# Kernel tuning notes

Measured on AMD Instinct MI355X. Metric: run time of the kernel, lower is better.

## Reference

```python
import jax, jax.numpy as jnp
import numpy as np

B, H, S, E = 16384, 16, 1, 64
N_OTHERS = 4


def setup_inputs() -> dict:
    key = jax.random.key(0)
    ks = jax.random.split(key, N_OTHERS + 2)
    inp = {f"others_{i}": jax.random.normal(ks[i], (B, H, S, E), dtype=jnp.float32)
           for i in range(N_OTHERS)}
    inp["main"] = jax.random.normal(ks[N_OTHERS], (B, H, S, E), dtype=jnp.float32)
    inp["W"] = jax.random.normal(ks[N_OTHERS + 1], (E, E), dtype=jnp.float32) * (1.0 / np.sqrt(E))
    return inp


def reference(others_0, others_1, others_2, others_3, main, W):
    # mean over the 'others' modalities: (B, H, 1, E)
    mean = (others_0 + others_1 + others_2 + others_3) / 4.0
    m = jnp.squeeze(mean, 2)        # (B, H, E)
    main_sq = jnp.squeeze(main, 2)  # (B, H, E)
    # bilinear score: mean @ W @ main^T -> (B, H, H)
    score = jnp.einsum('bhe,ef,bgf->bhg', m, W, main_sq)
    attn = jax.nn.softmax(score, axis=-1)      # (B, H, H)
    context = jnp.einsum('bhg,bge->bhe', attn, main_sq)  # (B, H, E)
    return context, attn
```

## Files before the change

kernel.cpp:

```cpp
#include <hip/hip_runtime.h>

#define NBATCH 16384
#define H 16
#define E 64
#define NB 4
#define NWAVE 4
#define NBLK (NBATCH / (NB * NWAVE))

#define LGKM0 do { asm volatile("s_waitcnt lgkmcnt(0)" ::: "memory"); \
                   __builtin_amdgcn_sched_barrier(0); } while (0)

__global__ __launch_bounds__(256, 3) void ovo_kernel(
    const float* __restrict__ o0, const float* __restrict__ o1,
    const float* __restrict__ o2, const float* __restrict__ o3,
    const float* __restrict__ mn, const float* __restrict__ W,
    float* __restrict__ ctx_out, float* __restrict__ attn_out)
{
    __shared__ float sW[E * E];
    __shared__ float sT[NWAVE][2][H * 68];

    const int tid = threadIdx.x;
    const int l   = tid & 63;
    const int wv  = tid >> 6;

#pragma unroll
    for (int c = 0; c < 4; ++c) {
        const int idx = c * 1024 + tid * 4;
        *(float4*)&sW[idx] = *(const float4*)&W[idx];
    }
    __syncthreads();

    float* const sA    = &sT[wv][0][0];
    float* const sMain = &sT[wv][1][0];

#pragma unroll 1
    for (int it = 0; it < NB; ++it) {
        const int batch = it * (NBLK * NWAVE) + blockIdx.x * NWAVE + wv;
        const size_t base = (size_t)batch * (H * E);

        float4 ra[4], rb[4], rc[4], rd[4], rv[4];
#pragma unroll
        for (int k = 0; k < 4; ++k) {
            const int off = k * 256 + l * 4;
            ra[k] = *(const float4*)(o0 + base + off);
            rb[k] = *(const float4*)(o1 + base + off);
            rc[k] = *(const float4*)(o2 + base + off);
            rd[k] = *(const float4*)(o3 + base + off);
            rv[k] = *(const float4*)(mn + base + off);
        }

#pragma unroll
        for (int k = 0; k < 4; ++k) {
            const int flat = k * 256 + l * 4;
            const int h = flat >> 6, e = flat & 63;
            float4 m4;
            m4.x = (ra[k].x + rb[k].x + rc[k].x + rd[k].x) * 0.25f;
            m4.y = (ra[k].y + rb[k].y + rc[k].y + rd[k].y) * 0.25f;
            m4.z = (ra[k].z + rb[k].z + rc[k].z + rd[k].z) * 0.25f;
            m4.w = (ra[k].w + rb[k].w + rc[k].w + rd[k].w) * 0.25f;
            *(float4*)&sA[h * 68 + e] = m4;
            *(float4*)&sMain[h * 68 + e] = rv[k];
        }
        LGKM0;

        {
            const int ht = l >> 4, ft = l & 15;
            const int h0 = ht * 4, f0 = ft * 4;
            float acc[4][4] = {{0.f}};
#pragma unroll
            for (int e0 = 0; e0 < 64; e0 += 4) {
                float4 mrow[4], wrow[4];
#pragma unroll
                for (int i = 0; i < 4; ++i) mrow[i] = *(const float4*)&sA[(h0 + i) * 68 + e0];
#pragma unroll
                for (int j = 0; j < 4; ++j) wrow[j] = *(const float4*)&sW[(e0 + j) * 64 + f0];
#pragma unroll
                for (int i = 0; i < 4; ++i) {
                    const float* mr = (const float*)&mrow[i];
#pragma unroll
                    for (int ee = 0; ee < 4; ++ee) {
                        const float* wr = (const float*)&wrow[ee];
#pragma unroll
                        for (int j = 0; j < 4; ++j)
                            acc[i][j] = fmaf(mr[ee], wr[j], acc[i][j]);
                    }
                }
            }
            LGKM0;
#pragma unroll
            for (int i = 0; i < 4; ++i)
                *(float4*)&sA[(h0 + i) * 68 + f0] =
                    make_float4(acc[i][0], acc[i][1], acc[i][2], acc[i][3]);
        }
        LGKM0;

        const int hp = l >> 2, gp = l & 3;
        const int g0 = gp * 4;
        float scr[4] = {0.f, 0.f, 0.f, 0.f};
#pragma unroll
        for (int f0 = 0; f0 < 64; f0 += 4) {
            float4 a0 = *(const float4*)&sA[hp * 68 + f0];
            const float* pa = (const float*)&a0;
            float4 b[4];
#pragma unroll
            for (int j = 0; j < 4; ++j)
                b[j] = *(const float4*)&sMain[(g0 + j) * 68 + f0];
#pragma unroll
            for (int j = 0; j < 4; ++j) {
                const float* pb = (const float*)&b[j];
#pragma unroll
                for (int q = 0; q < 4; ++q)
                    scr[j] = fmaf(pa[q], pb[q], scr[j]);
            }
        }
        LGKM0;

        {
            float mx = fmaxf(fmaxf(scr[0], scr[1]), fmaxf(scr[2], scr[3]));
            mx = fmaxf(mx, __shfl_xor(mx, 1));
            mx = fmaxf(mx, __shfl_xor(mx, 2));
            float e0 = __expf(scr[0] - mx), e1 = __expf(scr[1] - mx);
            float e2 = __expf(scr[2] - mx), e3 = __expf(scr[3] - mx);
            float sum = (e0 + e1) + (e2 + e3);
            sum += __shfl_xor(sum, 1);
            sum += __shfl_xor(sum, 2);
            const float inv = 1.0f / sum;
            float4 a4 = make_float4(e0 * inv, e1 * inv, e2 * inv, e3 * inv);
            *(float4*)(attn_out + (size_t)batch * (H * H) + l * 4) = a4;
            const float* pa4 = (const float*)&a4;
#pragma unroll
            for (int j = 0; j < 4; ++j)
                sA[(g0 + j) * 20 + hp] = pa4[j];
        }
        LGKM0;

        {
            const int ht = l >> 4, et = l & 15;
            const int h0 = ht * 4, e0c = et * 4;
            float acc[4][4] = {{0.f}};
#pragma unroll
            for (int g = 0; g < 16; ++g) {
                float4 bv = *(const float4*)&sMain[g * 68 + e0c];
                float4 av = *(const float4*)&sA[g * 20 + h0];
                const float* pb = (const float*)&bv;
                const float* pa = (const float*)&av;
#pragma unroll
                for (int i = 0; i < 4; ++i)
#pragma unroll
                    for (int j = 0; j < 4; ++j)
                        acc[i][j] = fmaf(pa[i], pb[j], acc[i][j]);
            }
            float* cp = ctx_out + base;
#pragma unroll
            for (int i = 0; i < 4; ++i)
                *(float4*)(cp + (h0 + i) * 64 + e0c) =
                    make_float4(acc[i][0], acc[i][1], acc[i][2], acc[i][3]);
        }
        LGKM0;
    }
}

extern "C" void kernel_launch(void* const* d_in, const int* in_sizes, int n_in,
                              void* d_out, int out_size, void* d_ws, size_t ws_size,
                              hipStream_t stream) {
    const float* o0 = (const float*)d_in[0];
    const float* o1 = (const float*)d_in[1];
    const float* o2 = (const float*)d_in[2];
    const float* o3 = (const float*)d_in[3];
    const float* mn = (const float*)d_in[4];
    const float* W  = (const float*)d_in[5];
    float* ctx  = (float*)d_out;
    float* attn = ctx + (size_t)NBATCH * H * E;
    hipLaunchKernelGGL(ovo_kernel, dim3(NBLK), dim3(NWAVE * 64), 0, stream,
                       o0, o1, o2, o3, mn, W, ctx, attn);
}
```

Measured before the change: 91.70 us.

## Compute mean@W with split-bf16 MFMA and load others directly into fragments

Replaces the scalar FMA 16x64x64 mean@W product with bf16 MFMA 16x16x32 instructions, using a hi/lo bf16 split (three products) to approximate fp32 accuracy. W is pre-split into bf16 fragment layout in LDS once per block. The others tensors are loaded straight into the MFMA A-fragment layout, so the mean no longer goes through LDS. A few lgkmcnt waits are also dropped. This trades some precision (the lo*lo term is omitted) and adds conversion work in exchange for fewer VALU FMAs.

```diff
diff --git a/kernel.cpp b/kernel.cpp
--- a/kernel.cpp
+++ b/kernel.cpp
@@ -6,6 +6,9 @@
 #define NB 4
 #define NWAVE 4
 #define NBLK (NBATCH / (NB * NWAVE))
+
+typedef __attribute__((ext_vector_type(8))) short short8v;
+typedef __attribute__((ext_vector_type(4))) float f32x4;
 
 #define LGKM0 do { asm volatile("s_waitcnt lgkmcnt(0)" ::: "memory"); \
                    __builtin_amdgcn_sched_barrier(0); } while (0)
@@ -16,81 +19,99 @@
     const float* __restrict__ mn, const float* __restrict__ W,
     float* __restrict__ ctx_out, float* __restrict__ attn_out)
 {
-    __shared__ float sW[E * E];
+    __shared__ __align__(16) unsigned short sWfrag[4][2][2][512];
     __shared__ float sT[NWAVE][2][H * 68];
 
     const int tid = threadIdx.x;
     const int l   = tid & 63;
     const int wv  = tid >> 6;
 
-#pragma unroll
-    for (int c = 0; c < 4; ++c) {
-        const int idx = c * 1024 + tid * 4;
-        *(float4*)&sW[idx] = *(const float4*)&W[idx];
+    for (int r = 0; r < 16; ++r) {
+        const int flat = r * 256 + tid;
+        const float w = W[flat];
+        const int e = flat >> 6, f = flat & 63;
+        const int t = f >> 4, col = f & 15;
+        const int s = e >> 5, khi = (e >> 3) & 3, i = e & 7;
+        const unsigned int wb = __float_as_uint(w);
+        const unsigned int hb = wb & 0xFFFF0000u;
+        const float lof = w - __uint_as_float(hb);
+        const unsigned int lb = __float_as_uint(lof);
+        const int L = col + 16 * khi;
+        sWfrag[t][s][0][L * 8 + i] = (unsigned short)(hb >> 16);
+        sWfrag[t][s][1][L * 8 + i] = (unsigned short)(lb >> 16);
     }
     __syncthreads();
 
-    float* const sA    = &sT[wv][0][0];
+    float* const sU    = &sT[wv][0][0];
     float* const sMain = &sT[wv][1][0];
+
+    const int q = l >> 4;
+    const int c = l & 15;
 
 #pragma unroll 1
     for (int it = 0; it < NB; ++it) {
         const int batch = it * (NBLK * NWAVE) + blockIdx.x * NWAVE + wv;
         const size_t base = (size_t)batch * (H * E);
 
-        float4 ra[4], rb[4], rc[4], rd[4], rv[4];
+        float4 mo[2][2];
 #pragma unroll
-        for (int k = 0; k < 4; ++k) {
-            const int off = k * 256 + l * 4;
-            ra[k] = *(const float4*)(o0 + base + off);
-            rb[k] = *(const float4*)(o1 + base + off);
-            rc[k] = *(const float4*)(o2 + base + off);
-            rd[k] = *(const float4*)(o3 + base + off);
-            rv[k] = *(const float4*)(mn + base + off);
-        }
+        for (int s = 0; s < 2; ++s)
+#pragma unroll
+            for (int c01 = 0; c01 < 2; ++c01) {
+                const size_t off = base + c * 64 + 32 * s + 8 * q + 4 * c01;
+                float4 a = *(const float4*)(o0 + off);
+                float4 b = *(const float4*)(o1 + off);
+                float4 g = *(const float4*)(o2 + off);
+                float4 d = *(const float4*)(o3 + off);
+                mo[s][c01].x = (a.x + b.x) + (g.x + d.x);
+                mo[s][c01].y = (a.y + b.y) + (g.y + d.y);
+                mo[s][c01].z = (a.z + b.z) + (g.z + d.z);
+                mo[s][c01].w = (a.w + b.w) + (g.w + d.w);
+            }
+        float4 rv[4];
+#pragma unroll
+        for (int k = 0; k < 4; ++k)
+            rv[k] = *(const float4*)(mn + base + k * 256 + l * 4);
 
 #pragma unroll
         for (int k = 0; k < 4; ++k) {
             const int flat = k * 256 + l * 4;
-            const int h = flat >> 6, e = flat & 63;
-            float4 m4;
-            m4.x = (ra[k].x + rb[k].x + rc[k].x + rd[k].x) * 0.25f;
-            m4.y = (ra[k].y + rb[k].y + rc[k].y + rd[k].y) * 0.25f;
-            m4.z = (ra[k].z + rb[k].z + rc[k].z + rd[k].z) * 0.25f;
-            m4.w = (ra[k].w + rb[k].w + rc[k].w + rd[k].w) * 0.25f;
-            *(float4*)&sA[h * 68 + e] = m4;
-            *(float4*)&sMain[h * 68 + e] = rv[k];
+            *(float4*)&sMain[(flat >> 6) * 68 + (flat & 63)] = rv[k];
         }
-        LGKM0;
 
-        {
-            const int ht = l >> 4, ft = l & 15;
-            const int h0 = ht * 4, f0 = ft * 4;
-            float acc[4][4] = {{0.f}};
+        short8v ahi[2], alo[2];
 #pragma unroll
-            for (int e0 = 0; e0 < 64; e0 += 4) {
-                float4 mrow[4], wrow[4];
+        for (int s = 0; s < 2; ++s) {
+            float ms[8];
+            ms[0] = mo[s][0].x; ms[1] = mo[s][0].y; ms[2] = mo[s][0].z; ms[3] = mo[s][0].w;
+            ms[4] = mo[s][1].x; ms[5] = mo[s][1].y; ms[6] = mo[s][1].z; ms[7] = mo[s][1].w;
 #pragma unroll
-                for (int i = 0; i < 4; ++i) mrow[i] = *(const float4*)&sA[(h0 + i) * 68 + e0];
+            for (int i = 0; i < 8; ++i) {
+                const float m = ms[i] * 0.25f;
+                const unsigned int mb = __float_as_uint(m);
+                const unsigned int hb = mb & 0xFFFF0000u;
+                const float lof = m - __uint_as_float(hb);
+                ahi[s][i] = (short)(hb >> 16);
+                alo[s][i] = (short)(__float_as_uint(lof) >> 16);
+            }
+        }
+
 #pragma unroll
-                for (int j = 0; j < 4; ++j) wrow[j] = *(const float4*)&sW[(e0 + j) * 64 + f0];
+        for (int t = 0; t < 4; ++t) {
+            short8v bh0 = *(const short8v*)&sWfrag[t][0][0][l * 8];
+            short8v bl0 = *(const short8v*)&sWfrag[t][0][1][l * 8];
+            short8v bh1 = *(const short8v*)&sWfrag[t][1][0][l * 8];
+            short8v bl1 = *(const short8v*)&sWfrag[t][1][1][l * 8];
+            f32x4 acc = {0.f, 0.f, 0.f, 0.f};
+            acc = __builtin_amdgcn_mfma_f32_16x16x32_bf16(ahi[0], bh0, acc, 0, 0, 0);
+            acc = __builtin_amdgcn_mfma_f32_16x16x32_bf16(alo[0], bh0, acc, 0, 0, 0);
+            acc = __builtin_amdgcn_mfma_f32_16x16x32_bf16(ahi[0], bl0, acc, 0, 0, 0);
+            acc = __builtin_amdgcn_mfma_f32_16x16x32_bf16(ahi[1], bh1, acc, 0, 0, 0);
+            acc = __builtin_amdgcn_mfma_f32_16x16x32_bf16(alo[1], bh1, acc, 0, 0, 0);
+            acc = __builtin_amdgcn_mfma_f32_16x16x32_bf16(ahi[1], bl1, acc, 0, 0, 0);
 #pragma unroll
-                for (int i = 0; i < 4; ++i) {
-                    const float* mr = (const float*)&mrow[i];
-#pragma unroll
-                    for (int ee = 0; ee < 4; ++ee) {
-                        const float* wr = (const float*)&wrow[ee];
-#pragma unroll
-                        for (int j = 0; j < 4; ++j)
-                            acc[i][j] = fmaf(mr[ee], wr[j], acc[i][j]);
-                    }
-                }
-            }
-            LGKM0;
-#pragma unroll
-            for (int i = 0; i < 4; ++i)
-                *(float4*)&sA[(h0 + i) * 68 + f0] =
-                    make_float4(acc[i][0], acc[i][1], acc[i][2], acc[i][3]);
+            for (int j = 0; j < 4; ++j)
+                sU[(4 * q + j) * 68 + 16 * t + c] = acc[j];
         }
         LGKM0;
 
@@ -99,7 +120,7 @@
         float scr[4] = {0.f, 0.f, 0.f, 0.f};
 #pragma unroll
         for (int f0 = 0; f0 < 64; f0 += 4) {
-            float4 a0 = *(const float4*)&sA[hp * 68 + f0];
+            float4 a0 = *(const float4*)&sU[hp * 68 + f0];
             const float* pa = (const float*)&a0;
             float4 b[4];
 #pragma unroll
@@ -109,11 +130,10 @@
             for (int j = 0; j < 4; ++j) {
                 const float* pb = (const float*)&b[j];
 #pragma unroll
-                for (int q = 0; q < 4; ++q)
-                    scr[j] = fmaf(pa[q], pb[q], scr[j]);
+                for (int u = 0; u < 4; ++u)
+                    scr[j] = fmaf(pa[u], pb[u], scr[j]);
             }
         }
-        LGKM0;
 
         {
             float mx = fmaxf(fmaxf(scr[0], scr[1]), fmaxf(scr[2], scr[3]));
@@ -130,33 +150,33 @@
             const float* pa4 = (const float*)&a4;
 #pragma unroll
             for (int j = 0; j < 4; ++j)
-                sA[(g0 + j) * 20 + hp] = pa4[j];
+                sU[(g0 + j) * 20 + hp] = pa4[j];
         }
         LGKM0;
 
         {
-            const int ht = l >> 4, et = l & 15;
+            const int ht = q, et = c;
             const int h0 = ht * 4, e0c = et * 4;
-            float acc[4][4] = {{0.f}};
+            f32x4 acc2[4] = {{0.f,0.f,0.f,0.f},{0.f,0.f,0.f,0.f},
+                             {0.f,0.f,0.f,0.f},{0.f,0.f,0.f,0.f}};
 #pragma unroll
             for (int g = 0; g < 16; ++g) {
                 float4 bv = *(const float4*)&sMain[g * 68 + e0c];
-                float4 av = *(const float4*)&sA[g * 20 + h0];
+                float4 av = *(const float4*)&sU[g * 20 + h0];
                 const float* pb = (const float*)&bv;
                 const float* pa = (const float*)&av;
 #pragma unroll
                 for (int i = 0; i < 4; ++i)
 #pragma unroll
                     for (int j = 0; j < 4; ++j)
-                        acc[i][j] = fmaf(pa[i], pb[j], acc[i][j]);
+                        acc2[i][j] = fmaf(pa[i], pb[j], acc2[i][j]);
             }
             float* cp = ctx_out + base;
 #pragma unroll
             for (int i = 0; i < 4; ++i)
                 *(float4*)(cp + (h0 + i) * 64 + e0c) =
-                    make_float4(acc[i][0], acc[i][1], acc[i][2], acc[i][3]);
+                    make_float4(acc2[i][0], acc2[i][1], acc2[i][2], acc2[i][3]);
         }
-        LGKM0;
     }
 }
 
```

After: 88.59 us. 3.4% less time.
